# Kernel optimization log

Hardware: AMD Instinct MI355X
Metric: run time of the kernel (lower is better)

Reference implementation:

```python
import jax, jax.numpy as jnp
import numpy as np

B, N, C, H, I, ID = 4, 1024, 1024, 16, 77, 768
HD = C // H
HID = 4 * C


def _ln(t, w, b):
    m = jnp.mean(t, axis=-1, keepdims=True)
    v = jnp.mean((t - m) ** 2, axis=-1, keepdims=True)
    return (t - m) * jax.lax.rsqrt(v + 1e-5) * w + b


def _gelu(t):
    return jax.nn.gelu(t, approximate=False)


def setup_inputs() -> dict:
    key = jax.random.key(0)
    ks = iter(jax.random.split(key, 16))

    def nrm(shape, s=0.02):
        return jax.random.normal(next(ks), shape, jnp.float32) * s

    return {
        'x': jax.random.normal(next(ks), (B, N, C), jnp.float32),
        'instruct_states': jax.random.normal(next(ks), (B, I, ID), jnp.float32),
        'norm1_w': jnp.ones((C,), jnp.float32), 'norm1_b': jnp.zeros((C,), jnp.float32),
        'qkv_w': nrm((3 * C, C)),
        'q_bias': jnp.zeros((C,), jnp.float32), 'v_bias': jnp.zeros((C,), jnp.float32),
        'proj_w': nrm((C, C)), 'proj_b': jnp.zeros((C,), jnp.float32),
        'gamma_1': jnp.full((C,), 1e-5, jnp.float32), 'gamma_2': jnp.full((C,), 1e-5, jnp.float32),
        'norm2_w': jnp.ones((C,), jnp.float32), 'norm2_b': jnp.zeros((C,), jnp.float32),
        'fc1_w': nrm((HID, C)), 'fc1_b': jnp.zeros((HID,), jnp.float32),
        'fc2_w': nrm((C, HID)), 'fc2_b': jnp.zeros((C,), jnp.float32),
        'pfc1_w': nrm((HID, C)), 'pfc1_b': jnp.zeros((HID,), jnp.float32),
        'pfc2_w': nrm((C, HID)), 'pfc2_b': jnp.zeros((C,), jnp.float32),
        'parallel_gate': jnp.full((1,), 0.1, jnp.float32),
        'ir_ln_w': jnp.ones((ID,), jnp.float32), 'ir_ln_b': jnp.zeros((ID,), jnp.float32),
        'ir_l1_w': nrm((C, ID)), 'ir_l1_b': jnp.zeros((C,), jnp.float32),
        'ir_l2_w': nrm((C, C)), 'ir_l2_b': jnp.zeros((C,), jnp.float32),
    }


def reference(x, instruct_states, norm1_w, norm1_b, qkv_w, q_bias, v_bias,
              proj_w, proj_b, gamma_1, gamma_2, norm2_w, norm2_b,
              fc1_w, fc1_b, fc2_w, fc2_b, pfc1_w, pfc1_b, pfc2_w, pfc2_b,
              parallel_gate, ir_ln_w, ir_ln_b, ir_l1_w, ir_l1_b, ir_l2_w, ir_l2_b):
    # instruct_dim_reduce: LN -> Linear -> GELU -> Linear
    kv = _ln(instruct_states, ir_ln_w, ir_ln_b)
    kv = _gelu(kv @ ir_l1_w.T + ir_l1_b) @ ir_l2_w.T + ir_l2_b  # [B, I, C]

    xn = _ln(x, norm1_w, norm1_b)                               # [B, N, C]
    cat = jnp.concatenate([kv, xn], axis=1)                     # [B, I+N, C]
    S = I + N

    qkv_bias = jnp.concatenate([q_bias, jnp.zeros_like(v_bias), v_bias])
    qkv = (cat @ qkv_w.T + qkv_bias).reshape(B, S, 3, H, HD)
    q = qkv[:, :, 0].transpose(0, 2, 1, 3)                      # [B, H, S, HD]
    k = qkv[:, :, 1].transpose(0, 2, 1, 3)
    v = qkv[:, :, 2].transpose(0, 2, 1, 3)

    # only visual queries, keys/values over instructions + visual tokens
    q = q[:, :, I:, :] * (HD ** -0.5)                           # [B, H, N, HD]
    attn = jnp.einsum('bhqd,bhkd->bhqk', q, k)                  # [B, H, N, S]
    attn = jax.nn.softmax(attn, axis=-1)
    o = jnp.einsum('bhqk,bhkd->bqhd', attn, v).reshape(B, N, C)
    o = o @ proj_w.T + proj_b

    x = x + gamma_1 * o                                         # LayerScale residual

    y = _ln(x, norm2_w, norm2_b)
    mlp = _gelu(y @ fc1_w.T + fc1_b) @ fc2_w.T + fc2_b
    pmlp = _gelu(y @ pfc1_w.T + pfc1_b) @ pfc2_w.T + pfc2_b
    x = x + gamma_2 * mlp + parallel_gate * pmlp
    return x
```

## Files before the change

### kernel.cpp

```cpp
#include <hip/hip_runtime.h>
#include <cstdint>

#define Bv   4
#define Nv   1024
#define Cv   1024
#define Hv   16
#define Iv   77
#define IDv  768
#define HDv  64
#define HIDv 4096
#define Sv   (Iv + Nv)
#define BIv  (Bv * Iv)
#define BSv  (Bv * Sv)
#define BNv  (Bv * Nv)
#define SPADv 1152

typedef __bf16 bf16x8_t __attribute__((ext_vector_type(8)));
typedef float  f32x4_t  __attribute__((ext_vector_type(4)));
typedef unsigned short us8_t __attribute__((ext_vector_type(8)));
typedef long  l2_t  __attribute__((ext_vector_type(2)));
typedef int   i32x4_t __attribute__((ext_vector_type(4)));
typedef int   i32x8_t __attribute__((ext_vector_type(8)));

__device__ inline f32x4_t zero4() { f32x4_t z; z[0]=0.f; z[1]=0.f; z[2]=0.f; z[3]=0.f; return z; }

__device__ inline unsigned short f2bf(float f) {
    unsigned int u = __builtin_bit_cast(unsigned int, f);
    u = (u + 0x7fffu + ((u >> 16) & 1u)) >> 16;
    return (unsigned short)u;
}
__device__ inline float bf2f(unsigned short u) {
    return __builtin_bit_cast(float, ((unsigned int)u) << 16);
}
__device__ inline unsigned int f4_fp8(float a, float b, float c, float d) {
    int v = __builtin_amdgcn_cvt_pk_fp8_f32(a, b, 0, false);
    v = __builtin_amdgcn_cvt_pk_fp8_f32(c, d, v, true);
    return (unsigned int)v;
}

__device__ inline float gelu_f(float x) {
    float u = 0.7978845608f * x * (1.0f + 0.044715f * x * x);
    float e = __expf(2.0f * u);
    float t = 1.0f - 2.0f / (e + 1.0f);
    return 0.5f * x * (1.0f + t);
}

__device__ inline void gload_lds16(const void* g, void* l) {
    __builtin_amdgcn_global_load_lds(
        (__attribute__((address_space(1))) void*)(unsigned long long)g,
        (__attribute__((address_space(3))) void*)(unsigned long long)l,
        16, 0, 0);
}

__device__ inline i32x8_t frag32(const unsigned char* p0, const unsigned char* p1) {
    i32x4_t lo = *(const i32x4_t*)p0;
    i32x4_t hi = *(const i32x4_t*)p1;
    i32x8_t r;
    r[0] = lo[0]; r[1] = lo[1]; r[2] = lo[2]; r[3] = lo[3];
    r[4] = hi[0]; r[5] = hi[1]; r[6] = hi[2]; r[7] = hi[3];
    return r;
}

__global__ __launch_bounds__(256) void cvt8_kernel(
        const float* s0, const float* s1, const float* s2, const float* s3,
        const float* s4, const float* s5, const float* s6, const float* s7,
        void* d0, void* d1, void* d2, void* d3,
        void* d4, void* d5, void* d6, void* d7,
        const float* g1, const float* g2, const float* gate) {
    long i = (long)blockIdx.x * 256 + threadIdx.x;
    const float* src; void* dst; long off;
    const float* sptr = nullptr; int K4 = 1; float wmul = 1.0f; bool f8 = false;
    if (i < 2097152) {
        if (i < 786432)       { src = s0; dst = d0; off = i; }
        else if (i < 1048576) { src = s1; dst = d1; off = i - 786432;  sptr = g1; K4 = 256; }
        else                  { src = s2; dst = d2; off = i - 1048576; f8 = true; wmul = 32.f; }
    } else if (i < 4194304) {
        if (i < 3145728)      { src = s3; dst = d3; off = i - 2097152; f8 = true; wmul = 32.f; sptr = g2; K4 = 1024; }
        else                  { src = s4; dst = d4; off = i - 3145728; f8 = true; wmul = 32.f; }
    } else {
        if (i < 5242880)      { src = s5; dst = d5; off = i - 4194304; f8 = true; wmul = 32.f; sptr = gate; K4 = 0x7fffffff; }
        else if (i < 5439488) { src = s6; dst = d6; off = i - 5242880; }
        else                  { src = s7; dst = d7; off = i - 5439488; }
    }
    float sc = (sptr ? sptr[(int)(off / K4)] : 1.0f) * wmul;
    float4 v = ((const float4*)src)[off];
    if (f8) {
        ((unsigned int*)dst)[off] = f4_fp8(v.x * sc, v.y * sc, v.z * sc, v.w * sc);
    } else {
        ushort4 o = {f2bf(v.x * sc), f2bf(v.y * sc), f2bf(v.z * sc), f2bf(v.w * sc)};
        ((ushort4*)dst)[off] = o;
    }
}

__global__ __launch_bounds__(256) void bias_prep_kernel(
        const float* __restrict__ qb, const float* __restrict__ vb,
        const float* __restrict__ fc2b, const float* __restrict__ pfc2b,
        const float* __restrict__ projb_in,
        const float* __restrict__ fc1b, const float* __restrict__ pfc1b,
        const float* __restrict__ g1, const float* __restrict__ g2,
        const float* __restrict__ gate,
        float* __restrict__ qkvb, float* __restrict__ bfuse,
        float* __restrict__ projb, float* __restrict__ bcat) {
    int i = blockIdx.x * 256 + threadIdx.x;
    if (i < 3 * Cv) {
        float v = 0.f;
        if (i < Cv) v = qb[i];
        else if (i >= 2 * Cv) v = vb[i - 2 * Cv];
        qkvb[i] = v;
    } else if (i < 4 * Cv) {
        int n = i - 3 * Cv;
        bfuse[n] = g2[n] * fc2b[n] + gate[0] * pfc2b[n];
    } else if (i < 5 * Cv) {
        int n = i - 4 * Cv;
        projb[n] = g1[n] * projb_in[n];
    } else if (i < 13 * Cv) {
        int j = i - 5 * Cv;
        bcat[j] = (j < HIDv) ? fc1b[j] : pfc1b[j - HIDv];
    }
}

__global__ __launch_bounds__(256) void scatter_kv_kernel(const unsigned short* __restrict__ kv,
                                                         unsigned short* __restrict__ cat) {
    int r = blockIdx.x;
    int b = r / Iv, i = r % Iv;
    const uint2* src = (const uint2*)(kv + (size_t)r * Cv);
    uint2* dst = (uint2*)(cat + (size_t)(b * Sv + i) * Cv);
    dst[threadIdx.x] = src[threadIdx.x];
}

template <int F8>
__global__ __launch_bounds__(256) void ln_kernel(const float* __restrict__ in,
                                                 const float* __restrict__ w,
                                                 const float* __restrict__ bvec,
                                                 void* __restrict__ out,
                                                 int cols, float invcols,
                                                 int div_, int stride_, int off_) {
    const int r = blockIdx.x;
    const int tid = threadIdx.x;
    const float* row = in + (size_t)r * cols;
    float s = 0.f, s2 = 0.f;
    for (int c = tid * 4; c < cols; c += 1024) {
        float4 v = *(const float4*)(row + c);
        s  += v.x + v.y + v.z + v.w;
        s2 += v.x * v.x + v.y * v.y + v.z * v.z + v.w * v.w;
    }
#pragma unroll
    for (int o2 = 32; o2 > 0; o2 >>= 1) { s += __shfl_down(s, o2); s2 += __shfl_down(s2, o2); }
    __shared__ float sh[10];
    const int lane = tid & 63, wave = tid >> 6;
    if (lane == 0) { sh[wave] = s; sh[4 + wave] = s2; }
    __syncthreads();
    if (tid == 0) {
        float S1 = sh[0] + sh[1] + sh[2] + sh[3];
        float S2 = sh[4] + sh[5] + sh[6] + sh[7];
        float mean = S1 * invcols;
        float var  = S2 * invcols - mean * mean;
        sh[8] = mean;
        sh[9] = rsqrtf(var + 1e-5f);
    }
    __syncthreads();
    const float mean = sh[8], rstd = sh[9];
    const size_t orow = (size_t)((r / div_) * stride_ + (r % div_) + off_) * cols;
    for (int c = tid * 4; c < cols; c += 1024) {
        float4 v  = *(const float4*)(row + c);
        float4 wv = *(const float4*)(w + c);
        float4 bv = *(const float4*)(bvec + c);
        float o0 = (v.x - mean) * rstd * wv.x + bv.x;
        float o1 = (v.y - mean) * rstd * wv.y + bv.y;
        float o2 = (v.z - mean) * rstd * wv.z + bv.z;
        float o3 = (v.w - mean) * rstd * wv.w + bv.w;
        if constexpr (F8) {
            *(unsigned int*)((unsigned char*)out + orow + c) =
                f4_fp8(o0 * 16.f, o1 * 16.f, o2 * 16.f, o3 * 16.f);
        } else {
            ushort4 o = {f2bf(o0), f2bf(o1), f2bf(o2), f2bf(o3)};
            *(ushort4*)((unsigned short*)out + orow + c) = o;
        }
    }
}

template <int MODE>
__global__ __launch_bounds__(256) void gemm_bf16_kernel(
        const unsigned short* __restrict__ A,
        const unsigned short* __restrict__ W,
        const float* __restrict__ bias,
        unsigned short* __restrict__ outp,
        int M, int N, int K) {
    __shared__ unsigned short As[2][128 * 32];
    __shared__ unsigned short Bs[2][128 * 32];
    const int tid  = threadIdx.x;
    const int lane = tid & 63;
    const int wave = tid >> 6;
    const int m16  = lane & 15;
    const int g4   = lane >> 4;
    const int n0 = blockIdx.x * 128;
    const int m0 = blockIdx.y * 128;
    const int wm = (wave >> 1) * 64;
    const int wn = (wave & 1) * 64;

    const int r0  = tid >> 2;
    const int cc0 = (tid & 3) * 8;
    int am0 = m0 + r0;       if (am0 > M - 1) am0 = M - 1;
    int am1 = m0 + r0 + 64;  if (am1 > M - 1) am1 = M - 1;
    const unsigned short* agp0 = A + (size_t)am0 * K + cc0;
    const unsigned short* agp1 = A + (size_t)am1 * K + cc0;
    const unsigned short* bgp0 = W + (size_t)(n0 + r0) * K + cc0;
    const unsigned short* bgp1 = W + (size_t)(n0 + r0 + 64) * K + cc0;

    f32x4_t acc[4][4];
#pragma unroll
    for (int a = 0; a < 4; ++a)
#pragma unroll
        for (int bb = 0; bb < 4; ++bb) acc[a][bb] = zero4();

    auto stage = [&](int buf) {
        gload_lds16(agp0, &As[buf][wave * 512]);
        gload_lds16(agp1, &As[buf][2048 + wave * 512]);
        gload_lds16(bgp0, &Bs[buf][wave * 512]);
        gload_lds16(bgp1, &Bs[buf][2048 + wave * 512]);
        agp0 += 32; agp1 += 32; bgp0 += 32; bgp1 += 32;
    };

    stage(0);
    const int NIT = K >> 5;
    for (int it = 0; it < NIT; ++it) {
        const int cur = it & 1;
        __syncthreads();
        if (it + 1 < NIT) stage(cur ^ 1);
        bf16x8_t xf[4], wf[4];
#pragma unroll
        for (int bb = 0; bb < 4; ++bb)
            xf[bb] = *(const bf16x8_t*)&As[cur][(wm + bb * 16 + m16) * 32 + g4 * 8];
#pragma unroll
        for (int a = 0; a < 4; ++a)
            wf[a] = *(const bf16x8_t*)&Bs[cur][(wn + a * 16 + m16) * 32 + g4 * 8];
#pragma unroll
        for (int a = 0; a < 4; ++a)
#pragma unroll
            for (int bb = 0; bb < 4; ++bb)
                acc[a][bb] = __builtin_amdgcn_mfma_f32_16x16x32_bf16(wf[a], xf[bb], acc[a][bb], 0, 0, 0);
    }

#pragma unroll
    for (int a = 0; a < 4; ++a) {
        const int cb = n0 + wn + a * 16 + g4 * 4;
        const float4 bv4 = *(const float4*)(bias + cb);
#pragma unroll
        for (int bb = 0; bb < 4; ++bb) {
            const int r = m0 + wm + bb * 16 + m16;
            if (r < M) {
                const size_t idx = (size_t)r * N + cb;
                const float v0 = acc[a][bb][0] + bv4.x;
                const float v1 = acc[a][bb][1] + bv4.y;
                const float v2 = acc[a][bb][2] + bv4.z;
                const float v3 = acc[a][bb][3] + bv4.w;
                if constexpr (MODE == 0) {
                    ushort4 o = {f2bf(v0), f2bf(v1), f2bf(v2), f2bf(v3)};
                    *(ushort4*)(outp + idx) = o;
                } else {
                    ushort4 o = {f2bf(gelu_f(v0)), f2bf(gelu_f(v1)),
                                 f2bf(gelu_f(v2)), f2bf(gelu_f(v3))};
                    *(ushort4*)(outp + idx) = o;
                }
            }
        }
    }
}

__global__ __launch_bounds__(256) void gemm_splitk_kernel(
        const unsigned short* __restrict__ A1,
        const unsigned short* __restrict__ W1,
        unsigned short* __restrict__ parts,
        int M, int N, int KA, int Kc) {
    __shared__ unsigned short As[2][128 * 32];
    __shared__ unsigned short Bs[2][128 * 32];
    const int tid  = threadIdx.x;
    const int lane = tid & 63;
    const int wave = tid >> 6;
    const int m16  = lane & 15;
    const int g4   = lane >> 4;
    const int bid = blockIdx.x;
    const int xcd = bid & 7, l = bid >> 3;
    const int by = (xcd << 2) | (l & 3);
    const int rr = l >> 2;
    const int bx = rr & 7;
    const int z  = rr >> 3;
    const int n0 = bx * 128;
    const int m0 = by * 128;
    const int wm = (wave >> 1) * 64;
    const int wn = (wave & 1) * 64;
    const int k0 = z * Kc;

    const int r0  = tid >> 2;
    const int cc0 = (tid & 3) * 8;
    const unsigned short* agp0 = A1 + (size_t)(m0 + r0) * KA + k0 + cc0;
    const unsigned short* agp1 = A1 + (size_t)(m0 + r0 + 64) * KA + k0 + cc0;
    const unsigned short* bgp0 = W1 + (size_t)(n0 + r0) * KA + k0 + cc0;
    const unsigned short* bgp1 = W1 + (size_t)(n0 + r0 + 64) * KA + k0 + cc0;

    f32x4_t acc[4][4];
#pragma unroll
    for (int a = 0; a < 4; ++a)
#pragma unroll
        for (int bb = 0; bb < 4; ++bb) acc[a][bb] = zero4();

    auto stage = [&](int buf) {
        gload_lds16(agp0, &As[buf][wave * 512]);
        gload_lds16(agp1, &As[buf][2048 + wave * 512]);
        gload_lds16(bgp0, &Bs[buf][wave * 512]);
        gload_lds16(bgp1, &Bs[buf][2048 + wave * 512]);
        agp0 += 32; agp1 += 32; bgp0 += 32; bgp1 += 32;
    };

    stage(0);
    const int NIT = Kc >> 5;
    for (int it = 0; it < NIT; ++it) {
        const int cur = it & 1;
        __syncthreads();
        if (it + 1 < NIT) stage(cur ^ 1);
        bf16x8_t xf[4], wf[4];
#pragma unroll
        for (int bb = 0; bb < 4; ++bb)
            xf[bb] = *(const bf16x8_t*)&As[cur][(wm + bb * 16 + m16) * 32 + g4 * 8];
#pragma unroll
        for (int a = 0; a < 4; ++a)
            wf[a] = *(const bf16x8_t*)&Bs[cur][(wn + a * 16 + m16) * 32 + g4 * 8];
#pragma unroll
        for (int a = 0; a < 4; ++a)
#pragma unroll
            for (int bb = 0; bb < 4; ++bb)
                acc[a][bb] = __builtin_amdgcn_mfma_f32_16x16x32_bf16(wf[a], xf[bb], acc[a][bb], 0, 0, 0);
    }

    unsigned short* pz = parts + (size_t)z * M * N;
#pragma unroll
    for (int a = 0; a < 4; ++a) {
        const int cb = n0 + wn + a * 16 + g4 * 4;
#pragma unroll
        for (int bb = 0; bb < 4; ++bb) {
            const int r = m0 + wm + bb * 16 + m16;
            const size_t idx = (size_t)r * N + cb;
            ushort4 o = {f2bf(acc[a][bb][0]), f2bf(acc[a][bb][1]),
                         f2bf(acc[a][bb][2]), f2bf(acc[a][bb][3])};
            *(ushort4*)(pz + idx) = o;
        }
    }
}

__global__ __launch_bounds__(256) void gemm_fp8_gelu_kernel(
        const unsigned char* __restrict__ A,
        const unsigned char* __restrict__ W,
        const float* __restrict__ bias,
        unsigned char* __restrict__ outp,
        int M, int N, int K) {
    __shared__ unsigned char As[2][128 * 128];
    __shared__ unsigned char Bs[2][128 * 128];
    const int tid  = threadIdx.x;
    const int lane = tid & 63;
    const int wave = tid >> 6;
    const int m16  = lane & 15;
    const int g4   = lane >> 4;
    const int bid = blockIdx.x;
    const int xcd = bid & 7, l = bid >> 3;
    const int by = (xcd << 2) | (l & 3);
    const int bx = l >> 2;
    const int n0 = bx * 128;
    const int m0 = by * 128;
    const int wm = (wave >> 1) * 64;
    const int wn = (wave & 1) * 64;

    const int rowin = tid >> 3;
    const int sslot = (tid & 7) ^ (rowin & 7);
    const unsigned char* agp = A + (size_t)(m0 + rowin) * K + sslot * 16;
    const unsigned char* bgp = W + (size_t)(n0 + rowin) * K + sslot * 16;

    const int sw = m16 & 7;
    const int ra0 = ((2 * g4) ^ sw) * 16;
    const int ra1 = ((2 * g4 + 1) ^ sw) * 16;

    f32x4_t acc[4][4];
#pragma unroll
    for (int a = 0; a < 4; ++a)
#pragma unroll
        for (int bb = 0; bb < 4; ++bb) acc[a][bb] = zero4();

    auto stage = [&](int buf) {
#pragma unroll
        for (int j = 0; j < 4; ++j) {
            gload_lds16(agp + (size_t)j * 32 * K, &As[buf][j * 4096 + wave * 1024]);
            gload_lds16(bgp + (size_t)j * 32 * K, &Bs[buf][j * 4096 + wave * 1024]);
        }
        agp += 128; bgp += 128;
    };

    stage(0);
    const int NIT = K >> 7;
    for (int it = 0; it < NIT; ++it) {
        const int cur = it & 1;
        __syncthreads();
        if (it + 1 < NIT) stage(cur ^ 1);
        i32x8_t xv[4], wv[4];
#pragma unroll
        for (int bb = 0; bb < 4; ++bb) {
            const unsigned char* rb = &As[cur][(wm + bb * 16 + m16) * 128];
            xv[bb] = frag32(rb + ra0, rb + ra1);
        }
#pragma unroll
        for (int a = 0; a < 4; ++a) {
            const unsigned char* rb = &Bs[cur][(wn + a * 16 + m16) * 128];
            wv[a] = frag32(rb + ra0, rb + ra1);
        }
#pragma unroll
        for (int a = 0; a < 4; ++a)
#pragma unroll
            for (int bb = 0; bb < 4; ++bb)
                acc[a][bb] = __builtin_amdgcn_mfma_scale_f32_16x16x128_f8f6f4(
                    wv[a], xv[bb], acc[a][bb], 0, 0, 0, 0x7f7f7f7f, 0, 0x7f7f7f7f);
    }

    const float ds = 1.0f / 512.0f;
#pragma unroll
    for (int a = 0; a < 4; ++a) {
        const int cb = n0 + wn + a * 16 + g4 * 4;
        const float4 bv4 = *(const float4*)(bias + cb);
#pragma unroll
        for (int bb = 0; bb < 4; ++bb) {
            const int r = m0 + wm + bb * 16 + m16;
            const size_t idx = (size_t)r * N + cb;
            unsigned int pk = f4_fp8(gelu_f(acc[a][bb][0] * ds + bv4.x) * 16.f,
                                     gelu_f(acc[a][bb][1] * ds + bv4.y) * 16.f,
                                     gelu_f(acc[a][bb][2] * ds + bv4.z) * 16.f,
                                     gelu_f(acc[a][bb][3] * ds + bv4.w) * 16.f);
            *(unsigned int*)(outp + idx) = pk;
        }
    }
}

__global__ __launch_bounds__(256) void gemm_fp8_splitk_kernel(
        const unsigned char* __restrict__ A1,
        const unsigned char* __restrict__ W1,
        const unsigned char* __restrict__ A2,
        const unsigned char* __restrict__ W2,
        unsigned short* __restrict__ parts,
        int M, int N, int lda, int ldw, int Kc, int zsplit) {
    __shared__ unsigned char As[2][128 * 128];
    __shared__ unsigned char Bs[2][128 * 128];
    const int tid  = threadIdx.x;
    const int lane = tid & 63;
    const int wave = tid >> 6;
    const int m16  = lane & 15;
    const int g4   = lane >> 4;
    const int bid = blockIdx.x;
    const int xcd = bid & 7, l = bid >> 3;
    const int by = (xcd << 2) | (l & 3);
    const int rr = l >> 2;
    const int bx = rr & 7;
    const int z  = rr >> 3;
    const int n0 = bx * 128;
    const int m0 = by * 128;
    const int wm = (wave >> 1) * 64;
    const int wn = (wave & 1) * 64;

    const unsigned char* A = (z < zsplit) ? A1 : A2;
    const unsigned char* W = (z < zsplit) ? W1 : W2;
    const int k0 = (z % zsplit) * Kc;

    const int rowin = tid >> 3;
    const int sslot = (tid & 7) ^ (rowin & 7);
    const unsigned char* agp = A + (size_t)(m0 + rowin) * lda + k0 + sslot * 16;
    const unsigned char* bgp = W + (size_t)(n0 + rowin) * ldw + k0 + sslot * 16;

    const int sw = m16 & 7;
    const int ra0 = ((2 * g4) ^ sw) * 16;
    const int ra1 = ((2 * g4 + 1) ^ sw) * 16;

    f32x4_t acc[4][4];
#pragma unroll
    for (int a = 0; a < 4; ++a)
#pragma unroll
        for (int bb = 0; bb < 4; ++bb) acc[a][bb] = zero4();

    auto stage = [&](int buf) {
#pragma unroll
        for (int j = 0; j < 4; ++j) {
            gload_lds16(agp + (size_t)j * 32 * lda, &As[buf][j * 4096 + wave * 1024]);
            gload_lds16(bgp + (size_t)j * 32 * ldw, &Bs[buf][j * 4096 + wave * 1024]);
        }
        agp += 128; bgp += 128;
    };

    stage(0);
    const int NIT = Kc >> 7;
    for (int it = 0; it < NIT; ++it) {
        const int cur = it & 1;
        __syncthreads();
        if (it + 1 < NIT) stage(cur ^ 1);
        i32x8_t xv[4], wv[4];
#pragma unroll
        for (int bb = 0; bb < 4; ++bb) {
            const unsigned char* rb = &As[cur][(wm + bb * 16 + m16) * 128];
            xv[bb] = frag32(rb + ra0, rb + ra1);
        }
#pragma unroll
        for (int a = 0; a < 4; ++a) {
            const unsigned char* rb = &Bs[cur][(wn + a * 16 + m16) * 128];
            wv[a] = frag32(rb + ra0, rb + ra1);
        }
#pragma unroll
        for (int a = 0; a < 4; ++a)
#pragma unroll
            for (int bb = 0; bb < 4; ++bb)
                acc[a][bb] = __builtin_amdgcn_mfma_scale_f32_16x16x128_f8f6f4(
                    wv[a], xv[bb], acc[a][bb], 0, 0, 0, 0x7f7f7f7f, 0, 0x7f7f7f7f);
    }

    unsigned short* pz = parts + (size_t)z * M * N;
    const float ds = 1.0f / 512.0f;
#pragma unroll
    for (int a = 0; a < 4; ++a) {
        const int cb = n0 + wn + a * 16 + g4 * 4;
#pragma unroll
        for (int bb = 0; bb < 4; ++bb) {
            const int r = m0 + wm + bb * 16 + m16;
            const size_t idx = (size_t)r * N + cb;
            ushort4 o = {f2bf(acc[a][bb][0] * ds), f2bf(acc[a][bb][1] * ds),
                         f2bf(acc[a][bb][2] * ds), f2bf(acc[a][bb][3] * ds)};
            *(ushort4*)(pz + idx) = o;
        }
    }
}

template <int NP>
__global__ __launch_bounds__(256) void reduce_kernel(
        const unsigned short* __restrict__ parts,
        const float* __restrict__ resid,
        const float* __restrict__ bias,
        float* __restrict__ out, int MN, int N4mask) {
    int i = blockIdx.x * 256 + threadIdx.x;
    if (i * 4 >= MN) return;
    float4 res = ((const float4*)resid)[i];
    float4 bv  = *(const float4*)(bias + (i & N4mask) * 4);
    float4 o = {res.x + bv.x, res.y + bv.y, res.z + bv.z, res.w + bv.w};
#pragma unroll
    for (int z = 0; z < NP; ++z) {
        ushort4 u = ((const ushort4*)(parts + (size_t)z * MN))[i];
        o.x += bf2f(u.x); o.y += bf2f(u.y); o.z += bf2f(u.z); o.w += bf2f(u.w);
    }
    ((float4*)out)[i] = o;
}

__global__ __launch_bounds__(256) void vtrans_kernel(const unsigned short* __restrict__ qkv,
                                                     unsigned short* __restrict__ vt) {
    __shared__ unsigned short Vs[64 * 64];
    const int stile = blockIdx.x;
    const int bh = blockIdx.y;
    const int b = bh >> 4, h = bh & 15;
    const int tid = threadIdx.x;
#pragma unroll
    for (int j = 0; j < 2; ++j) {
        int c = j * 256 + tid;
        int r = c >> 3, d8 = (c & 7) * 8;
        int s = stile * 64 + r;
        uint4 v = {0u, 0u, 0u, 0u};
        if (s < Sv) v = *(const uint4*)(qkv + ((size_t)(b * Sv + s) * 3 + 2) * Cv + h * 64 + d8);
        *(uint4*)&Vs[r * 64 + d8] = v;
    }
    __syncthreads();
    const int d  = tid >> 2;
    const int p0 = (tid & 3) * 16;
    unsigned short tmp[16];
#pragma unroll
    for (int e = 0; e < 16; ++e) {
        int p = p0 + e;
        int s_local = (p & 32) + 16 * ((p >> 2) & 1) + 4 * ((p & 31) >> 3) + (p & 3);
        tmp[e] = Vs[s_local * 64 + d];
    }
    unsigned short* dst = vt + ((size_t)bh * 64 + d) * SPADv + stile * 64 + p0;
    *(uint4*)dst       = *(const uint4*)&tmp[0];
    *(uint4*)(dst + 8) = *(const uint4*)&tmp[8];
}

__global__ __launch_bounds__(256) void attn_kernel(const unsigned short* __restrict__ qkv,
                                                   const unsigned short* __restrict__ vt,
                                                   unsigned short* __restrict__ o) {
    __shared__ unsigned short Qs[64 * 64];
    __shared__ unsigned short Ks[2][64 * 64];
    __shared__ unsigned short Vts[2][64 * 64];

    const int tid  = threadIdx.x;
    const int lane = tid & 63;
    const int wave = tid >> 6;
    const int m16  = lane & 15;
    const int g4   = lane >> 4;
    const int qt = blockIdx.x;
    const int bh = blockIdx.y;
    const int b = bh >> 4, h = bh & 15;

    const int lr = lane >> 3;
    const int csw = ((lane & 7) ^ lr) * 8;
    const int sw7 = m16 & 7;

#pragma unroll
    for (int j = 0; j < 2; ++j) {
        int r = wave * 16 + j * 8 + lr;
        int s = Iv + qt * 64 + r;
        gload_lds16(qkv + ((size_t)(b * Sv + s) * 3) * Cv + h * 64 + csw,
                    &Qs[(wave * 16 + j * 8) * 64]);
    }

    auto stage_kv = [&](int st, int buf) {
#pragma unroll
        for (int j = 0; j < 2; ++j) {
            int r = wave * 16 + j * 8 + lr;
            int s = st * 64 + r; if (s > Sv - 1) s = Sv - 1;
            gload_lds16(qkv + ((size_t)(b * Sv + s) * 3 + 1) * Cv + h * 64 + csw,
                        &Ks[buf][(wave * 16 + j * 8) * 64]);
            gload_lds16(vt + ((size_t)bh * 64 + r) * SPADv + st * 64 + csw,
                        &Vts[buf][(wave * 16 + j * 8) * 64]);
        }
    };

    f32x4_t oacc[4];
#pragma unroll
    for (int dt = 0; dt < 4; ++dt) oacc[dt] = zero4();
    float m_run = -1e30f, l_run = 0.f;

    stage_kv(0, 0);
    __syncthreads();

    const bf16x8_t qf0 = *(const bf16x8_t*)&Qs[(wave * 16 + m16) * 64 + ((g4 ^ sw7) * 8)];
    const bf16x8_t qf1 = *(const bf16x8_t*)&Qs[(wave * 16 + m16) * 64 + (((4 + g4) ^ sw7) * 8)];

    const int NT = (Sv + 63) / 64;
    for (int st = 0; st < NT; ++st) {
        const int cur = st & 1;
        if (st + 1 < NT) stage_kv(st + 1, cur ^ 1);

        f32x4_t sc[4];
#pragma unroll
        for (int kt = 0; kt < 4; ++kt) {
            bf16x8_t k0 = *(const bf16x8_t*)&Ks[cur][(kt * 16 + m16) * 64 + ((g4 ^ sw7) * 8)];
            bf16x8_t k1 = *(const bf16x8_t*)&Ks[cur][(kt * 16 + m16) * 64 + (((4 + g4) ^ sw7) * 8)];
            f32x4_t z = zero4();
            z = __builtin_amdgcn_mfma_f32_16x16x32_bf16(k0, qf0, z, 0, 0, 0);
            z = __builtin_amdgcn_mfma_f32_16x16x32_bf16(k1, qf1, z, 0, 0, 0);
            sc[kt] = z;
        }

        float mx = -1e30f;
#pragma unroll
        for (int kt = 0; kt < 4; ++kt)
#pragma unroll
            for (int r = 0; r < 4; ++r) {
                int key = st * 64 + kt * 16 + g4 * 4 + r;
                float v = sc[kt][r] * 0.125f;
                v = (key < Sv) ? v : -1e30f;
                sc[kt][r] = v;
                mx = fmaxf(mx, v);
            }
        mx = fmaxf(mx, __shfl_xor(mx, 16));
        mx = fmaxf(mx, __shfl_xor(mx, 32));
        const float mnew  = fmaxf(m_run, mx);
        const float alpha = __expf(m_run - mnew);
        m_run = mnew;
        float sum = 0.f;
#pragma unroll
        for (int kt = 0; kt < 4; ++kt)
#pragma unroll
            for (int r = 0; r < 4; ++r) {
                float p = __expf(sc[kt][r] - mnew);
                sc[kt][r] = p;
                sum += p;
            }
        sum += __shfl_xor(sum, 16);
        sum += __shfl_xor(sum, 32);
        l_run = l_run * alpha + sum;
#pragma unroll
        for (int dt = 0; dt < 4; ++dt) oacc[dt] *= alpha;

        us8_t pu0, pu1;
#pragma unroll
        for (int j = 0; j < 8; ++j) {
            pu0[j] = f2bf(sc[(j >> 2)][j & 3]);
            pu1[j] = f2bf(sc[2 + (j >> 2)][j & 3]);
        }
        const bf16x8_t pf0 = __builtin_bit_cast(bf16x8_t, pu0);
        const bf16x8_t pf1 = __builtin_bit_cast(bf16x8_t, pu1);

#pragma unroll
        for (int dt = 0; dt < 4; ++dt) {
            bf16x8_t v0 = *(const bf16x8_t*)&Vts[cur][(dt * 16 + m16) * 64 + ((g4 ^ sw7) * 8)];
            bf16x8_t v1 = *(const bf16x8_t*)&Vts[cur][(dt * 16 + m16) * 64 + (((4 + g4) ^ sw7) * 8)];
            oacc[dt] = __builtin_amdgcn_mfma_f32_16x16x32_bf16(v0, pf0, oacc[dt], 0, 0, 0);
            oacc[dt] = __builtin_amdgcn_mfma_f32_16x16x32_bf16(v1, pf1, oacc[dt], 0, 0, 0);
        }
        __syncthreads();
    }

    const float inv = 1.0f / l_run;
    const int q = qt * 64 + wave * 16 + m16;
    const size_t row = (size_t)(b * Nv + q) * Cv + h * 64;
#pragma unroll
    for (int dt = 0; dt < 4; ++dt) {
        ushort4 o4 = {f2bf(oacc[dt][0] * inv), f2bf(oacc[dt][1] * inv),
                      f2bf(oacc[dt][2] * inv), f2bf(oacc[dt][3] * inv)};
        *(ushort4*)&o[row + dt * 16 + g4 * 4] = o4;
    }
}

extern "C" void kernel_launch(void* const* d_in, const int* in_sizes, int n_in,
                              void* d_out, int out_size, void* d_ws, size_t ws_size,
                              hipStream_t stream) {
    (void)in_sizes; (void)n_in; (void)out_size; (void)ws_size;
    const float* x       = (const float*)d_in[0];
    const float* instr   = (const float*)d_in[1];
    const float* norm1_w = (const float*)d_in[2];
    const float* norm1_b = (const float*)d_in[3];
    const float* qkv_w   = (const float*)d_in[4];
    const float* q_bias  = (const float*)d_in[5];
    const float* v_bias  = (const float*)d_in[6];
    const float* proj_w  = (const float*)d_in[7];
    const float* proj_b  = (const float*)d_in[8];
    const float* gamma_1 = (const float*)d_in[9];
    const float* gamma_2 = (const float*)d_in[10];
    const float* norm2_w = (const float*)d_in[11];
    const float* norm2_b = (const float*)d_in[12];
    const float* fc1_w   = (const float*)d_in[13];
    const float* fc1_b   = (const float*)d_in[14];
    const float* fc2_w   = (const float*)d_in[15];
    const float* fc2_b   = (const float*)d_in[16];
    const float* pfc1_w  = (const float*)d_in[17];
    const float* pfc1_b  = (const float*)d_in[18];
    const float* pfc2_w  = (const float*)d_in[19];
    const float* pfc2_b  = (const float*)d_in[20];
    const float* gate    = (const float*)d_in[21];
    const float* ir_ln_w = (const float*)d_in[22];
    const float* ir_ln_b = (const float*)d_in[23];
    const float* ir_l1_w = (const float*)d_in[24];
    const float* ir_l1_b = (const float*)d_in[25];
    const float* ir_l2_w = (const float*)d_in[26];
    const float* ir_l2_b = (const float*)d_in[27];
    float* out = (float*)d_out;

    char* ws = (char*)d_ws;
    size_t off = 0;
    auto alloc = [&](size_t bytes) -> char* {
        char* p = ws + off;
        off += (bytes + 255) & ~(size_t)255;
        return p;
    };
    unsigned short* w_qkv  = (unsigned short*)alloc((size_t)3 * Cv * Cv * 2);
    unsigned short* w_proj = (unsigned short*)alloc((size_t)Cv * Cv * 2);
    unsigned char*  w_mlp1 = (unsigned char*)alloc((size_t)2 * HIDv * Cv);
    unsigned char*  w_fc2  = (unsigned char*)alloc((size_t)Cv * HIDv);
    unsigned char*  w_pfc2 = (unsigned char*)alloc((size_t)Cv * HIDv);
    unsigned short* w_ir1  = (unsigned short*)alloc((size_t)Cv * IDv * 2);
    unsigned short* w_ir2  = (unsigned short*)alloc((size_t)Cv * Cv * 2);
    float*          qkvb   = (float*)alloc((size_t)3 * Cv * 4);
    float*          bfuse  = (float*)alloc((size_t)Cv * 4);
    float*          projb  = (float*)alloc((size_t)Cv * 4);
    float*          bcat   = (float*)alloc((size_t)2 * HIDv * 4);
    unsigned short* irln   = (unsigned short*)alloc((size_t)BIv * IDv * 2);
    unsigned short* h1     = (unsigned short*)alloc((size_t)BIv * Cv * 2);
    unsigned short* kvtmp  = (unsigned short*)alloc((size_t)BIv * Cv * 2);
    unsigned short* cat    = (unsigned short*)alloc((size_t)BSv * Cv * 2);
    unsigned short* qkvbuf = (unsigned short*)alloc((size_t)BSv * 3 * Cv * 2);
    unsigned short* obuf   = (unsigned short*)alloc((size_t)BNv * Cv * 2);
    float*          x1     = (float*)alloc((size_t)BNv * Cv * 4);
    unsigned char*  ybuf8  = (unsigned char*)alloc((size_t)BNv * Cv);
    unsigned char*  gbufA  = (unsigned char*)alloc((size_t)BNv * 2 * HIDv);
    unsigned short* fpart  = (unsigned short*)alloc((size_t)4 * BNv * Cv * 2);
    unsigned short* vt     = (unsigned short*)gbufA;
    unsigned short* ppart  = cat;

    cvt8_kernel<<<22272, 256, 0, stream>>>(qkv_w, proj_w, fc1_w, fc2_w, pfc1_w, pfc2_w,
                                           ir_l1_w, ir_l2_w,
                                           w_qkv, w_proj, w_mlp1, w_fc2,
                                           w_mlp1 + (size_t)HIDv * Cv, w_pfc2,
                                           w_ir1, w_ir2,
                                           gamma_1, gamma_2, gate);

    bias_prep_kernel<<<52, 256, 0, stream>>>(q_bias, v_bias, fc2_b, pfc2_b, proj_b,
                                             fc1_b, pfc1_b,
                                             gamma_1, gamma_2, gate,
                                             qkvb, bfuse, projb, bcat);

    ln_kernel<0><<<BIv, 256, 0, stream>>>(instr, ir_ln_w, ir_ln_b, irln,
                                          IDv, 1.0f / IDv, 1 << 28, 0, 0);
    ln_kernel<0><<<BNv, 256, 0, stream>>>(x, norm1_w, norm1_b, cat,
                                          Cv, 1.0f / Cv, Nv, Sv, Iv);
    gemm_bf16_kernel<1><<<dim3(Cv / 128, (BIv + 127) / 128), 256, 0, stream>>>(
        irln, w_ir1, ir_l1_b, h1, BIv, Cv, IDv);
    gemm_bf16_kernel<0><<<dim3(Cv / 128, (BIv + 127) / 128), 256, 0, stream>>>(
        h1, w_ir2, ir_l2_b, kvtmp, BIv, Cv, Cv);
    scatter_kv_kernel<<<BIv, 256, 0, stream>>>(kvtmp, cat);

    gemm_bf16_kernel<0><<<dim3(3 * Cv / 128, (BSv + 127) / 128), 256, 0, stream>>>(
        cat, w_qkv, qkvb, qkvbuf, BSv, 3 * Cv, Cv);

    vtrans_kernel<<<dim3(18, Bv * Hv), 256, 0, stream>>>(qkvbuf, vt);
    attn_kernel<<<dim3(Nv / 64, Bv * Hv), 256, 0, stream>>>(qkvbuf, vt, obuf);

    gemm_splitk_kernel<<<1024, 256, 0, stream>>>(
        obuf, w_proj, ppart, BNv, Cv, Cv, Cv / 4);
    reduce_kernel<4><<<(BNv * Cv / 4 + 255) / 256, 256, 0, stream>>>(
        ppart, x, projb, x1, BNv * Cv, Cv / 4 - 1);

    ln_kernel<1><<<BNv, 256, 0, stream>>>(x1, norm2_w, norm2_b, ybuf8,
                                          Cv, 1.0f / Cv, 1 << 28, 0, 0);

    gemm_fp8_gelu_kernel<<<2048, 256, 0, stream>>>(
        ybuf8, w_mlp1, bcat, gbufA, BNv, 2 * HIDv, Cv);

    gemm_fp8_splitk_kernel<<<1024, 256, 0, stream>>>(
        gbufA, w_fc2, gbufA + HIDv, w_pfc2, fpart,
        BNv, Cv, 2 * HIDv, HIDv, HIDv / 2, 2);
    reduce_kernel<4><<<(BNv * Cv / 4 + 255) / 256, 256, 0, stream>>>(
        fpart, x1, bfuse, out, BNv * Cv, Cv / 4 - 1);
}
```

Measured before the change: 482.4 us.

## Restructure GEMM main loops to keep two LDS stages in flight with vmcnt waits

All four GEMM kernels (bf16 and fp8, plain and split-K) now issue two global-to-LDS stages before the loop. Each iteration waits with a partial s_waitcnt vmcnt so only the current buffer's loads must finish, then computes and refills that buffer after a second barrier. This replaces the __syncthreads-then-prefetch pattern, so loads for the next tile are already outstanding during compute and the full memory drain per iteration goes away. It adds an extra barrier per iteration and relies on hand-counted vmcnt values matching the number of outstanding load instructions.

```diff
diff --git a/kernel.cpp b/kernel.cpp
--- a/kernel.cpp
+++ b/kernel.cpp
@@ -60,6 +60,16 @@
     r[4] = hi[0]; r[5] = hi[1]; r[6] = hi[2]; r[7] = hi[3];
     return r;
 }
+
+#define PIPE_WAIT(N) do { \
+    asm volatile("s_waitcnt vmcnt(" #N ")" ::: "memory"); \
+    __builtin_amdgcn_s_barrier(); \
+    __builtin_amdgcn_sched_barrier(0); \
+} while (0)
+#define PIPE_RELEASE() do { \
+    __builtin_amdgcn_sched_barrier(0); \
+    __builtin_amdgcn_s_barrier(); \
+} while (0)
 
 __global__ __launch_bounds__(256) void cvt8_kernel(
         const float* s0, const float* s1, const float* s2, const float* s3,
@@ -221,12 +231,7 @@
         agp0 += 32; agp1 += 32; bgp0 += 32; bgp1 += 32;
     };
 
-    stage(0);
-    const int NIT = K >> 5;
-    for (int it = 0; it < NIT; ++it) {
-        const int cur = it & 1;
-        __syncthreads();
-        if (it + 1 < NIT) stage(cur ^ 1);
+    auto body = [&](int cur) {
         bf16x8_t xf[4], wf[4];
 #pragma unroll
         for (int bb = 0; bb < 4; ++bb)
@@ -239,7 +244,20 @@
 #pragma unroll
             for (int bb = 0; bb < 4; ++bb)
                 acc[a][bb] = __builtin_amdgcn_mfma_f32_16x16x32_bf16(wf[a], xf[bb], acc[a][bb], 0, 0, 0);
-    }
+    };
+
+    const int NIT = K >> 5;
+    stage(0);
+    stage(1);
+    for (int it = 0; it < NIT - 1; ++it) {
+        const int cur = it & 1;
+        PIPE_WAIT(4);
+        body(cur);
+        PIPE_RELEASE();
+        if (it + 2 < NIT) stage(cur);
+    }
+    PIPE_WAIT(0);
+    body((NIT - 1) & 1);
 
 #pragma unroll
     for (int a = 0; a < 4; ++a) {
@@ -312,12 +330,7 @@
         agp0 += 32; agp1 += 32; bgp0 += 32; bgp1 += 32;
     };
 
-    stage(0);
-    const int NIT = Kc >> 5;
-    for (int it = 0; it < NIT; ++it) {
-        const int cur = it & 1;
-        __syncthreads();
-        if (it + 1 < NIT) stage(cur ^ 1);
+    auto body = [&](int cur) {
         bf16x8_t xf[4], wf[4];
 #pragma unroll
         for (int bb = 0; bb < 4; ++bb)
@@ -330,7 +343,20 @@
 #pragma unroll
             for (int bb = 0; bb < 4; ++bb)
                 acc[a][bb] = __builtin_amdgcn_mfma_f32_16x16x32_bf16(wf[a], xf[bb], acc[a][bb], 0, 0, 0);
-    }
+    };
+
+    const int NIT = Kc >> 5;
+    stage(0);
+    stage(1);
+    for (int it = 0; it < NIT - 1; ++it) {
+        const int cur = it & 1;
+        PIPE_WAIT(4);
+        body(cur);
+        PIPE_RELEASE();
+        if (it + 2 < NIT) stage(cur);
+    }
+    PIPE_WAIT(0);
+    body((NIT - 1) & 1);
 
     unsigned short* pz = parts + (size_t)z * M * N;
 #pragma unroll
@@ -393,12 +419,7 @@
         agp += 128; bgp += 128;
     };
 
-    stage(0);
-    const int NIT = K >> 7;
-    for (int it = 0; it < NIT; ++it) {
-        const int cur = it & 1;
-        __syncthreads();
-        if (it + 1 < NIT) stage(cur ^ 1);
+    auto body = [&](int cur) {
         i32x8_t xv[4], wv[4];
 #pragma unroll
         for (int bb = 0; bb < 4; ++bb) {
@@ -416,7 +437,20 @@
             for (int bb = 0; bb < 4; ++bb)
                 acc[a][bb] = __builtin_amdgcn_mfma_scale_f32_16x16x128_f8f6f4(
                     wv[a], xv[bb], acc[a][bb], 0, 0, 0, 0x7f7f7f7f, 0, 0x7f7f7f7f);
-    }
+    };
+
+    const int NIT = K >> 7;
+    stage(0);
+    stage(1);
+    for (int it = 0; it < NIT - 1; ++it) {
+        const int cur = it & 1;
+        PIPE_WAIT(8);
+        body(cur);
+        PIPE_RELEASE();
+        if (it + 2 < NIT) stage(cur);
+    }
+    PIPE_WAIT(0);
+    body((NIT - 1) & 1);
 
     const float ds = 1.0f / 512.0f;
 #pragma unroll
@@ -489,12 +523,7 @@
         agp += 128; bgp += 128;
     };
 
-    stage(0);
-    const int NIT = Kc >> 7;
-    for (int it = 0; it < NIT; ++it) {
-        const int cur = it & 1;
-        __syncthreads();
-        if (it + 1 < NIT) stage(cur ^ 1);
+    auto body = [&](int cur) {
         i32x8_t xv[4], wv[4];
 #pragma unroll
         for (int bb = 0; bb < 4; ++bb) {
@@ -512,7 +541,20 @@
             for (int bb = 0; bb < 4; ++bb)
                 acc[a][bb] = __builtin_amdgcn_mfma_scale_f32_16x16x128_f8f6f4(
                     wv[a], xv[bb], acc[a][bb], 0, 0, 0, 0x7f7f7f7f, 0, 0x7f7f7f7f);
-    }
+    };
+
+    const int NIT = Kc >> 7;
+    stage(0);
+    stage(1);
+    for (int it = 0; it < NIT - 1; ++it) {
+        const int cur = it & 1;
+        PIPE_WAIT(8);
+        body(cur);
+        PIPE_RELEASE();
+        if (it + 2 < NIT) stage(cur);
+    }
+    PIPE_WAIT(0);
+    body((NIT - 1) & 1);
 
     unsigned short* pz = parts + (size_t)z * M * N;
     const float ds = 1.0f / 512.0f;
```

After: 479.5 us. No clear change (-0.6%).
